# Optimization experiments

Hardware: AMD Instinct MI355X
Metric: run time of the kernel (lower is better)

Reference implementation:

```python
import jax, jax.numpy as jnp
import numpy as np

EMBED_DIM = 768
NUM_HEADS = 12


def setup_inputs() -> dict:
    key = jax.random.key(0)
    ks = jax.random.split(key, 9)
    C = EMBED_DIM
    x = jax.random.normal(ks[0], (8, 3136, C), dtype=jnp.float32)
    s = 0.02
    Wq = jax.random.normal(ks[1], (C, C), dtype=jnp.float32) * s
    Wk = jax.random.normal(ks[2], (C, C), dtype=jnp.float32) * s
    Wv = jax.random.normal(ks[3], (C, C), dtype=jnp.float32) * s
    Wo = jax.random.normal(ks[4], (C, C), dtype=jnp.float32) * s
    bq = jax.random.normal(ks[5], (C,), dtype=jnp.float32) * s
    bk = jax.random.normal(ks[6], (C,), dtype=jnp.float32) * s
    bv = jax.random.normal(ks[7], (C,), dtype=jnp.float32) * s
    bo = jax.random.normal(ks[8], (C,), dtype=jnp.float32) * s
    return {"x": x, "Wq": Wq, "bq": bq, "Wk": Wk, "bk": bk,
            "Wv": Wv, "bv": bv, "Wo": Wo, "bo": bo, "T": 16}


def reference(x, Wq, bq, Wk, bk, Wv, bv, Wo, bo, T):
    B, N, C = x.shape
    H = NUM_HEADS
    hd = C // H
    Hh = H // 2
    P = N // T
    scale = 1.0 / np.sqrt(hd).astype(np.float32)

    Q = (x @ Wq + bq).reshape(B, T, P, H, hd)
    K = (x @ Wk + bk).reshape(B, T, P, H, hd)
    V = (x @ Wv + bv).reshape(B, T, P, H, hd)

    # spatial attention: first Hh heads, attend over patches within each frame
    Qs, Ks, Vs = Q[..., :Hh, :], K[..., :Hh, :], V[..., :Hh, :]
    scores_s = jnp.einsum('btphd,btqhd->bthpq', Qs, Ks) * scale  # (B,T,Hh,P,P)
    ws = jax.nn.softmax(scores_s, axis=-1)
    out_s = jnp.einsum('bthpq,btqhd->btphd', ws, Vs)  # (B,T,P,Hh,hd)

    # temporal attention: last Hh heads, attend over frames at each patch
    Qt, Kt, Vt = Q[..., Hh:, :], K[..., Hh:, :], V[..., Hh:, :]
    scores_t = jnp.einsum('btphd,bsphd->bphts', Qt, Kt) * scale  # (B,P,Hh,T,T)
    wt = jax.nn.softmax(scores_t, axis=-1)
    out_t = jnp.einsum('bphts,bsphd->btphd', wt, Vt)  # (B,T,P,Hh,hd)

    out = jnp.concatenate([out_s, out_t], axis=3).reshape(B, N, C)
    return out @ Wo + bo
```

## Files before the change

### kernel.cpp

```cpp
#include <hip/hip_runtime.h>


typedef __attribute__((ext_vector_type(8))) short short8;
typedef __attribute__((ext_vector_type(4))) float f32x4;

typedef __attribute__((address_space(1))) void gvoid;
typedef __attribute__((address_space(3))) void lvoid;

__device__ __forceinline__ unsigned short f2b(float f) {
  unsigned int u = __float_as_uint(f);
  unsigned int r = (u + 0x7FFFu + ((u >> 16) & 1u)) >> 16;
  return (unsigned short)r;
}

__global__ __launch_bounds__(256) void k_prep(
    const float* __restrict__ x, unsigned short* __restrict__ xb,
    const float* __restrict__ bq, const float* __restrict__ bk,
    const float* __restrict__ bv, float* __restrict__ bqkv,
    const float* __restrict__ Wq, const float* __restrict__ Wk,
    const float* __restrict__ Wv, const float* __restrict__ Wo,
    unsigned short* __restrict__ wqkvT, unsigned short* __restrict__ woT) {
  __shared__ float tile[32][33];
  if (blockIdx.x < 18816) {
    int tid = blockIdx.x * 256 + threadIdx.x;
    if (tid < 2304)
      bqkv[tid] = tid < 768 ? bq[tid] : (tid < 1536 ? bk[tid - 768] : bv[tid - 1536]);
    float4 v = ((const float4*)x)[tid];
    ushort4 o;
    o.x = f2b(v.x); o.y = f2b(v.y); o.z = f2b(v.z); o.w = f2b(v.w);
    ((ushort4*)xb)[tid] = o;
    return;
  }
  int bid = blockIdx.x - 18816;
  const float* W;
  unsigned short* dst;
  int n0, k0;
  if (bid < 1728) {
    int tn = bid % 72, tk = bid / 72;
    n0 = tn * 32; k0 = tk * 32;
    int which = n0 / 768;
    W = which == 0 ? Wq : (which == 1 ? Wk : Wv);
    dst = wqkvT;
  } else {
    int b2 = bid - 1728;
    int tn = b2 % 24, tk = b2 / 24;
    n0 = tn * 32; k0 = tk * 32;
    W = Wo; dst = woT;
  }
  int nn0 = n0 % 768;
  for (int i = threadIdx.x; i < 1024; i += 256) {
    int r = i >> 5, c = i & 31;
    tile[r][c] = W[(size_t)(k0 + r) * 768 + nn0 + c];
  }
  __syncthreads();
  for (int i = threadIdx.x; i < 1024; i += 256) {
    int r = i >> 5, c = i & 31;
    dst[(size_t)(n0 + r) * 768 + k0 + c] = f2b(tile[c][r]);
  }
}


#define FENCE asm volatile("" ::: "memory")
#define BARRIER do { FENCE; __builtin_amdgcn_s_barrier(); FENCE; } while (0)
#define WAIT_LGKM0 asm volatile("s_waitcnt lgkmcnt(0)" ::: "memory")
#define WAIT_VM4 asm volatile("s_waitcnt vmcnt(4)" ::: "memory")

#define STAGE(PBASE, BUFBASE, HT, KT_) do {                                          \
    int kt__ = (KT_);                                                                \
    bool real__ = (kt__ < 12);                                                       \
    if (!real__) kt__ -= 12;                                                         \
    const unsigned short* src__ = (PBASE) + (HT) * 98304 + kt__ * 64;                \
    unsigned d0__ = real__ ? ((BUFBASE) + (HT) * 8192 + w * 512) : (65536u + w * 512); \
    unsigned d1__ = real__ ? ((BUFBASE) + (HT) * 8192 + 4096 + w * 512) : (65536u + w * 512); \
    __builtin_amdgcn_global_load_lds((const gvoid*)src__, (lvoid*)(lds + d0__), 16, 0, 0); \
    __builtin_amdgcn_global_load_lds((const gvoid*)(src__ + 49152), (lvoid*)(lds + d1__), 16, 0, 0); \
  } while (0)

#define LDA(MH, ABASE) do {                                                          \
    const unsigned short* ab__ = lds + (ABASE) + ((MH) * 128 + arow) * 64;           \
    _Pragma("unroll")                                                                \
    for (int mf = 0; mf < 4; ++mf) {                                                 \
      af[mf][0] = *(const short8*)(ab__ + mf * 1024 + s0);                           \
      af[mf][1] = *(const short8*)(ab__ + mf * 1024 + s1);                           \
    }                                                                                \
  } while (0)

#define LDB(NH, BBASE) do {                                                          \
    const unsigned short* bb__ = lds + (BBASE) + ((NH) * 128 + brow) * 64;           \
    _Pragma("unroll")                                                                \
    for (int nf = 0; nf < 2; ++nf) {                                                 \
      bf[nf][0] = *(const short8*)(bb__ + nf * 1024 + s0);                           \
      bf[nf][1] = *(const short8*)(bb__ + nf * 1024 + s1);                           \
    }                                                                                \
  } while (0)

#define MM(MH, NH) do {                                                              \
    __builtin_amdgcn_s_setprio(1);                                                   \
    _Pragma("unroll")                                                                \
    for (int mf = 0; mf < 4; ++mf) {                                                 \
      _Pragma("unroll")                                                              \
      for (int nf = 0; nf < 2; ++nf) {                                               \
        acc[MH][mf][NH][nf] = __builtin_amdgcn_mfma_f32_16x16x32_bf16(               \
            af[mf][0], bf[nf][0], acc[MH][mf][NH][nf], 0, 0, 0);                     \
        acc[MH][mf][NH][nf] = __builtin_amdgcn_mfma_f32_16x16x32_bf16(               \
            af[mf][1], bf[nf][1], acc[MH][mf][NH][nf], 0, 0, 0);                     \
      }                                                                              \
    }                                                                                \
    __builtin_amdgcn_s_setprio(0);                                                   \
  } while (0)

__global__ __launch_bounds__(512, 2) void k_gemm256(
    const unsigned short* __restrict__ A, const unsigned short* __restrict__ Bt,
    const float* __restrict__ bias, unsigned short* __restrict__ Cout,
    int M, int N) {
  __shared__ __align__(16) unsigned short lds[69632];
  const int nwg = gridDim.x;
  const int nbx = N >> 8;
  const int orig = blockIdx.x;
  const int q = nwg >> 3, r = nwg & 7;
  const int xcd = orig & 7, lin = orig >> 3;
  const int wg = (xcd < r ? xcd * (q + 1) : r * (q + 1) + (xcd - r) * q) + lin;
  const int m0 = (wg / nbx) << 8, n0 = (wg % nbx) << 8;

  const int tid = threadIdx.x;
  const int w = tid >> 6, l = tid & 63;
  const int wm = w >> 2, wn = w & 3;
  const int lg = l >> 4, ln = l & 15;
  const int arow = wm * 64 + ln;
  const int brow = wn * 32 + ln;
  const int s0 = (lg ^ (ln & 7)) * 8;
  const int s1 = s0 ^ 32;
  const int srow = tid >> 3;
  const int slg8 = ((tid & 7) ^ (srow & 7)) * 8;
  const unsigned short* pA = A + (size_t)(m0 + srow) * 768 + slg8;
  const unsigned short* pB = Bt + (size_t)(n0 + srow) * 768 + slg8;

  f32x4 acc[2][4][2][2] = {};

  STAGE(pA, 0,     0, 0);
  STAGE(pB, 16384, 0, 0);
  STAGE(pA, 0,     1, 0);
  STAGE(pB, 16384, 1, 0);
  STAGE(pA, 32768, 0, 1);
  STAGE(pB, 49152, 1, 1);
  WAIT_VM4;
  BARRIER;

  for (int it = 0; it < 6; ++it) {
    const int kt1 = 2 * it + 1, ktn0 = 2 * it + 2, ktn1 = 2 * it + 3;
    short8 af[4][2], bf[2][2];
    LDA(0, 0); LDB(0, 16384);
    STAGE(pA, 32768, 1, kt1);
    BARRIER; WAIT_LGKM0; MM(0, 0);
    LDB(1, 16384);
    STAGE(pB, 49152, 0, kt1);
    BARRIER; WAIT_LGKM0; MM(0, 1);
    LDA(1, 0);
    STAGE(pA, 0, 0, ktn0);
    BARRIER; WAIT_LGKM0; MM(1, 1);
    LDB(0, 16384);
    STAGE(pB, 16384, 1, ktn0);
    WAIT_VM4;
    BARRIER; WAIT_LGKM0; MM(1, 0);
    LDA(0, 32768); LDB(0, 49152);
    STAGE(pA, 0, 1, ktn0);
    BARRIER; WAIT_LGKM0; MM(0, 0);
    LDB(1, 49152);
    STAGE(pB, 16384, 0, ktn0);
    BARRIER; WAIT_LGKM0; MM(0, 1);
    LDA(1, 32768);
    STAGE(pA, 32768, 0, ktn1);
    BARRIER; WAIT_LGKM0; MM(1, 1);
    LDB(0, 49152);
    STAGE(pB, 49152, 1, ktn1);
    WAIT_VM4;
    BARRIER; WAIT_LGKM0; MM(1, 0);
  }

#pragma unroll
  for (int mh = 0; mh < 2; ++mh)
#pragma unroll
    for (int mf = 0; mf < 4; ++mf)
#pragma unroll
      for (int nh = 0; nh < 2; ++nh)
#pragma unroll
        for (int nf = 0; nf < 2; ++nf) {
          const int col = n0 + nh * 128 + wn * 32 + nf * 16 + ln;
          const float bval = bias[col];
          const int row = m0 + mh * 128 + wm * 64 + mf * 16 + lg * 4;
#pragma unroll
          for (int rr = 0; rr < 4; ++rr)
            Cout[(size_t)(row + rr) * N + col] = f2b(acc[mh][mf][nh][nf][rr] + bval);
        }
}

__global__ __launch_bounds__(256) void k_gemm_out(
    const unsigned short* __restrict__ A, const unsigned short* __restrict__ Bt,
    const float* __restrict__ bias, float* __restrict__ C,
    int M, int N, int K) {
  __shared__ __align__(16) unsigned short As[2][128 * 32];
  __shared__ __align__(16) unsigned short Bs[2][128 * 32];
  const int tid = threadIdx.x;
  const int w = tid >> 6, l = tid & 63;
  const int lg = l >> 4, ln = l & 15;
  const int m0 = blockIdx.y * 128, n0 = blockIdx.x * 128;
  const int wr = (w >> 1) * 64, wc = (w & 1) * 64;
  f32x4 acc[4][4] = {};
  const unsigned short* ga = A + (size_t)(m0 + (tid >> 2)) * K + ((tid & 3) * 8);
  const unsigned short* gb = Bt + (size_t)(n0 + (tid >> 2)) * K + ((tid & 3) * 8);
  const size_t krow64 = (size_t)64 * K;
  const int wofs = w * 512;

#define OSTAGE(CO, K0) do {                                                                        \
    __builtin_amdgcn_global_load_lds((const gvoid*)(ga + (K0)),          (lvoid*)(&As[0][0] + (CO) + wofs),        16, 0, 0); \
    __builtin_amdgcn_global_load_lds((const gvoid*)(ga + krow64 + (K0)), (lvoid*)(&As[0][0] + (CO) + 2048 + wofs), 16, 0, 0); \
    __builtin_amdgcn_global_load_lds((const gvoid*)(gb + (K0)),          (lvoid*)(&Bs[0][0] + (CO) + wofs),        16, 0, 0); \
    __builtin_amdgcn_global_load_lds((const gvoid*)(gb + krow64 + (K0)), (lvoid*)(&Bs[0][0] + (CO) + 2048 + wofs), 16, 0, 0); \
  } while (0)

  OSTAGE(0, 0);
  asm volatile("s_waitcnt vmcnt(0)" ::: "memory");
  BARRIER;
  int co = 0;
  for (int k0 = 0; k0 < K; k0 += 32) {
    if (k0 + 32 < K) OSTAGE(co ^ 4096, k0 + 32);
    const unsigned short* as = &As[0][0] + co;
    const unsigned short* bs = &Bs[0][0] + co;
    short8 a[4], b[4];
#pragma unroll
    for (int mt = 0; mt < 4; ++mt)
      a[mt] = *(const short8*)(as + (wr + mt * 16 + ln) * 32 + lg * 8);
#pragma unroll
    for (int nt = 0; nt < 4; ++nt)
      b[nt] = *(const short8*)(bs + (wc + nt * 16 + ln) * 32 + lg * 8);
#pragma unroll
    for (int mt = 0; mt < 4; ++mt)
#pragma unroll
      for (int nt = 0; nt < 4; ++nt)
        acc[mt][nt] = __builtin_amdgcn_mfma_f32_16x16x32_bf16(a[mt], b[nt], acc[mt][nt], 0, 0, 0);
    asm volatile("s_waitcnt vmcnt(0)" ::: "memory");
    BARRIER;
    co ^= 4096;
  }
#pragma unroll
  for (int nt = 0; nt < 4; ++nt) {
    int col = n0 + wc + nt * 16 + ln;
    float bval = bias[col];
#pragma unroll
    for (int mt = 0; mt < 4; ++mt) {
      int row = m0 + wr + mt * 16 + lg * 4;
#pragma unroll
      for (int r = 0; r < 4; ++r)
        C[(size_t)(row + r) * N + col] = acc[mt][nt][r] + bval;
    }
  }
#undef OSTAGE
}

__global__ __launch_bounds__(256) void k_attn_fused(
    const unsigned short* __restrict__ qkv, unsigned short* __restrict__ attn) {
  __shared__ __align__(16) unsigned short smem[29696];
  const int w = threadIdx.x >> 6, l = threadIdx.x & 63;
  const int lg = l >> 4, ln = l & 15;
  const float scale = 0.125f;
  if (blockIdx.x < 768) {
    const int bi = blockIdx.x;
    const int h = bi % 6;
    const int t = (bi / 6) % 16;
    const int b = bi / 96;
    const int base_row = b * 3136 + t * 196;
    unsigned short* Vt = smem;
    unsigned short* Pl = smem + 14848;
    for (int i = threadIdx.x; i < 196 * 8; i += 256) {
      int key = i >> 3, d0 = (i & 7) * 8;
      short8 v = *(const short8*)(qkv + (size_t)(base_row + key) * 2304 + 1536 + h * 64 + d0);
#pragma unroll
      for (int j = 0; j < 8; ++j) Vt[(d0 + j) * 232 + key] = (unsigned short)v[j];
    }
    for (int i = threadIdx.x; i < 64 * 28; i += 256)
      Vt[(i / 28) * 232 + 196 + (i % 28)] = 0;
    __syncthreads();
    for (int mt = w; mt < 13; mt += 4) {
      int qm = mt * 16 + ln; if (qm > 195) qm = 195;
      const size_t qoff = (size_t)(base_row + qm) * 2304 + h * 64 + lg * 8;
      short8 qa0 = *(const short8*)(qkv + qoff);
      short8 qa1 = *(const short8*)(qkv + qoff + 32);
      f32x4 st[13];
#pragma unroll
      for (int nt = 0; nt < 13; ++nt) {
        int kn = nt * 16 + ln; if (kn > 195) kn = 195;
        const size_t koff = (size_t)(base_row + kn) * 2304 + 768 + h * 64 + lg * 8;
        short8 kb0 = *(const short8*)(qkv + koff);
        short8 kb1 = *(const short8*)(qkv + koff + 32);
        f32x4 s = {0.f, 0.f, 0.f, 0.f};
        s = __builtin_amdgcn_mfma_f32_16x16x32_bf16(qa0, kb0, s, 0, 0, 0);
        s = __builtin_amdgcn_mfma_f32_16x16x32_bf16(qa1, kb1, s, 0, 0, 0);
        st[nt] = s;
      }
      float mr[4] = {-1e30f, -1e30f, -1e30f, -1e30f};
#pragma unroll
      for (int nt = 0; nt < 13; ++nt) {
        bool valid = (nt * 16 + ln) < 196;
#pragma unroll
        for (int r = 0; r < 4; ++r) {
          float v = valid ? st[nt][r] * scale : -1e30f;
          st[nt][r] = v;
          mr[r] = fmaxf(mr[r], v);
        }
      }
#pragma unroll
      for (int msk = 1; msk <= 8; msk <<= 1)
#pragma unroll
        for (int r = 0; r < 4; ++r) mr[r] = fmaxf(mr[r], __shfl_xor(mr[r], msk));
      float sm[4] = {0.f, 0.f, 0.f, 0.f};
#pragma unroll
      for (int nt = 0; nt < 13; ++nt)
#pragma unroll
        for (int r = 0; r < 4; ++r) {
          float p = __expf(st[nt][r] - mr[r]);
          st[nt][r] = p;
          sm[r] += p;
        }
#pragma unroll
      for (int msk = 1; msk <= 8; msk <<= 1)
#pragma unroll
        for (int r = 0; r < 4; ++r) sm[r] += __shfl_xor(sm[r], msk);
      float inv[4];
#pragma unroll
      for (int r = 0; r < 4; ++r) inv[r] = 1.f / sm[r];
      unsigned short* Pw = Pl + w * 16 * 232;
#pragma unroll
      for (int nt = 0; nt < 13; ++nt)
#pragma unroll
        for (int r = 0; r < 4; ++r)
          Pw[(lg * 4 + r) * 232 + nt * 16 + ln] = f2b(st[nt][r] * inv[r]);
#pragma unroll
      for (int r = 0; r < 4; ++r) Pw[ln * 232 + 208 + lg * 4 + r] = 0;
#pragma unroll
      for (int nt4 = 0; nt4 < 4; ++nt4) {
        f32x4 acc = {0.f, 0.f, 0.f, 0.f};
#pragma unroll
        for (int ks = 0; ks < 7; ++ks) {
          short8 pa = *(const short8*)(Pw + ln * 232 + ks * 32 + lg * 8);
          short8 vb = *(const short8*)(Vt + (nt4 * 16 + ln) * 232 + ks * 32 + lg * 8);
          acc = __builtin_amdgcn_mfma_f32_16x16x32_bf16(pa, vb, acc, 0, 0, 0);
        }
#pragma unroll
        for (int r = 0; r < 4; ++r) {
          int m = mt * 16 + lg * 4 + r;
          if (m < 196)
            attn[(size_t)(base_row + m) * 768 + h * 64 + nt4 * 16 + ln] = f2b(acc[r]);
        }
      }
    }
  } else {
    const int u = (blockIdx.x - 768) * 4 + w;
    const int b = u / 1176;
    const int rem = u % 1176;
    const int p = rem / 6;
    const int h = 6 + rem % 6;
    const size_t rowb = (size_t)b * 3136 + p;
    unsigned short* Vt = smem + w * 2560;
    unsigned short* Pl = smem + 10240 + w * 640;
    for (int i = l; i < 128; i += 64) {
      int tt = i >> 3, d0 = (i & 7) * 8;
      short8 v = *(const short8*)(qkv + (rowb + (size_t)tt * 196) * 2304 + 1536 + h * 64 + d0);
#pragma unroll
      for (int j = 0; j < 8; ++j) Vt[(d0 + j) * 40 + tt] = (unsigned short)v[j];
    }
    for (int i = l; i < 1024; i += 64)
      Vt[(i >> 4) * 40 + 16 + (i & 15)] = 0;
    const size_t qoff = (rowb + (size_t)ln * 196) * 2304 + h * 64 + lg * 8;
    short8 qa0 = *(const short8*)(qkv + qoff);
    short8 qa1 = *(const short8*)(qkv + qoff + 32);
    short8 kb0 = *(const short8*)(qkv + qoff + 768);
    short8 kb1 = *(const short8*)(qkv + qoff + 768 + 32);
    f32x4 s = {0.f, 0.f, 0.f, 0.f};
    s = __builtin_amdgcn_mfma_f32_16x16x32_bf16(qa0, kb0, s, 0, 0, 0);
    s = __builtin_amdgcn_mfma_f32_16x16x32_bf16(qa1, kb1, s, 0, 0, 0);
    float stv[4], mr[4];
#pragma unroll
    for (int r = 0; r < 4; ++r) { stv[r] = s[r] * scale; mr[r] = stv[r]; }
#pragma unroll
    for (int msk = 1; msk <= 8; msk <<= 1)
#pragma unroll
      for (int r = 0; r < 4; ++r) mr[r] = fmaxf(mr[r], __shfl_xor(mr[r], msk));
    float sm[4];
#pragma unroll
    for (int r = 0; r < 4; ++r) { stv[r] = __expf(stv[r] - mr[r]); sm[r] = stv[r]; }
#pragma unroll
    for (int msk = 1; msk <= 8; msk <<= 1)
#pragma unroll
      for (int r = 0; r < 4; ++r) sm[r] += __shfl_xor(sm[r], msk);
#pragma unroll
    for (int r = 0; r < 4; ++r)
      Pl[(lg * 4 + r) * 40 + ln] = f2b(stv[r] / sm[r]);
#pragma unroll
    for (int r = 0; r < 4; ++r) Pl[ln * 40 + 16 + lg * 4 + r] = 0;
    short8 pa = *(const short8*)(Pl + ln * 40 + lg * 8);
#pragma unroll
    for (int nt4 = 0; nt4 < 4; ++nt4) {
      short8 vb = *(const short8*)(Vt + (nt4 * 16 + ln) * 40 + lg * 8);
      f32x4 acc = {0.f, 0.f, 0.f, 0.f};
      acc = __builtin_amdgcn_mfma_f32_16x16x32_bf16(pa, vb, acc, 0, 0, 0);
#pragma unroll
      for (int r = 0; r < 4; ++r) {
        int tq = lg * 4 + r;
        attn[((size_t)b * 3136 + (size_t)tq * 196 + p) * 768 + h * 64 + nt4 * 16 + ln] = f2b(acc[r]);
      }
    }
  }
}

extern "C" void kernel_launch(void* const* d_in, const int* in_sizes, int n_in,
                              void* d_out, int out_size, void* d_ws, size_t ws_size,
                              hipStream_t stream) {
  const float* x  = (const float*)d_in[0];
  const float* Wq = (const float*)d_in[1];
  const float* bq = (const float*)d_in[2];
  const float* Wk = (const float*)d_in[3];
  const float* bk = (const float*)d_in[4];
  const float* Wv = (const float*)d_in[5];
  const float* bv = (const float*)d_in[6];
  const float* Wo = (const float*)d_in[7];
  const float* bo = (const float*)d_in[8];
  float* out = (float*)d_out;
  char* ws = (char*)d_ws;
  unsigned short* xb    = (unsigned short*)(ws + 0);
  unsigned short* wqkvT = (unsigned short*)(ws + 38535168);
  float*          bqkv  = (float*)(ws + 42074112);
  unsigned short* woT   = (unsigned short*)(ws + 42083328);
  unsigned short* qkvb  = (unsigned short*)(ws + 43262976);
  unsigned short* attnb = (unsigned short*)(ws + 158868480);

  k_prep<<<21120, 256, 0, stream>>>(x, xb, bq, bk, bv, bqkv, Wq, Wk, Wv, Wo, wqkvT, woT);
  k_gemm256<<<882, 512, 0, stream>>>(xb, wqkvT, bqkv, qkvb, 25088, 2304);
  k_attn_fused<<<3120, 256, 0, stream>>>(qkvb, attnb);
  k_gemm_out<<<dim3(6, 196), 256, 0, stream>>>(attnb, woT, bo, out, 25088, 768, 768);
}
```

Baseline: 248.3 us.

## Keep softmax probabilities in registers by transposing QK^T and permuting V layout

Computes S^T (K as the A operand, Q as the B operand) so each lane's MFMA accumulator maps directly onto the A-operand register layout of the PV MFMA. V columns in shared memory are permuted to match that layout. This removes the shared-memory round trip for P and halves the kernel's LDS footprint. It also drops the max subtraction from softmax and defers normalization to the output, which saves the reductions but risks overflow in exp when scores are large.

```diff
diff --git a/kernel.cpp b/kernel.cpp
--- a/kernel.cpp
+++ b/kernel.cpp
@@ -1,8 +1,10 @@
 #include <hip/hip_runtime.h>
+#include <hip/hip_bf16.h>
 
 
 typedef __attribute__((ext_vector_type(8))) short short8;
 typedef __attribute__((ext_vector_type(4))) float f32x4;
+typedef __attribute__((ext_vector_type(4))) unsigned int u32x4;
 
 typedef __attribute__((address_space(1))) void gvoid;
 typedef __attribute__((address_space(3))) void lvoid;
@@ -11,6 +13,18 @@
   unsigned int u = __float_as_uint(f);
   unsigned int r = (u + 0x7FFFu + ((u >> 16) & 1u)) >> 16;
   return (unsigned short)r;
+}
+
+__device__ __forceinline__ unsigned int pk2(float a, float b) {
+  union { __hip_bfloat162 h; unsigned int u; } cv;
+  cv.h = __float22bfloat162_rn(float2{a, b});
+  return cv.u;
+}
+
+__device__ __forceinline__ int vperm(int key) {
+  int u = key & 31;
+  return (key & ~31) | (((u >> 3) & 1) << 4) | (((u >> 2) & 1) << 3) |
+         (((u >> 4) & 1) << 2) | (u & 3);
 }
 
 __global__ __launch_bounds__(256) void k_prep(
@@ -259,7 +273,7 @@
 
 __global__ __launch_bounds__(256) void k_attn_fused(
     const unsigned short* __restrict__ qkv, unsigned short* __restrict__ attn) {
-  __shared__ __align__(16) unsigned short smem[29696];
+  __shared__ __align__(16) unsigned short smem[14848];
   const int w = threadIdx.x >> 6, l = threadIdx.x & 63;
   const int lg = l >> 4, ln = l & 15;
   const float scale = 0.125f;
@@ -270,12 +284,12 @@
     const int b = bi / 96;
     const int base_row = b * 3136 + t * 196;
     unsigned short* Vt = smem;
-    unsigned short* Pl = smem + 14848;
     for (int i = threadIdx.x; i < 196 * 8; i += 256) {
       int key = i >> 3, d0 = (i & 7) * 8;
       short8 v = *(const short8*)(qkv + (size_t)(base_row + key) * 2304 + 1536 + h * 64 + d0);
-#pragma unroll
-      for (int j = 0; j < 8; ++j) Vt[(d0 + j) * 232 + key] = (unsigned short)v[j];
+      int col = vperm(key);
+#pragma unroll
+      for (int j = 0; j < 8; ++j) Vt[(d0 + j) * 232 + col] = (unsigned short)v[j];
     }
     for (int i = threadIdx.x; i < 64 * 28; i += 256)
       Vt[(i / 28) * 232 + 196 + (i % 28)] = 0;
@@ -283,73 +297,63 @@
     for (int mt = w; mt < 13; mt += 4) {
       int qm = mt * 16 + ln; if (qm > 195) qm = 195;
       const size_t qoff = (size_t)(base_row + qm) * 2304 + h * 64 + lg * 8;
-      short8 qa0 = *(const short8*)(qkv + qoff);
-      short8 qa1 = *(const short8*)(qkv + qoff + 32);
+      short8 qb0 = *(const short8*)(qkv + qoff);
+      short8 qb1 = *(const short8*)(qkv + qoff + 32);
       f32x4 st[13];
 #pragma unroll
       for (int nt = 0; nt < 13; ++nt) {
         int kn = nt * 16 + ln; if (kn > 195) kn = 195;
         const size_t koff = (size_t)(base_row + kn) * 2304 + 768 + h * 64 + lg * 8;
-        short8 kb0 = *(const short8*)(qkv + koff);
-        short8 kb1 = *(const short8*)(qkv + koff + 32);
+        short8 ka0 = *(const short8*)(qkv + koff);
+        short8 ka1 = *(const short8*)(qkv + koff + 32);
         f32x4 s = {0.f, 0.f, 0.f, 0.f};
-        s = __builtin_amdgcn_mfma_f32_16x16x32_bf16(qa0, kb0, s, 0, 0, 0);
-        s = __builtin_amdgcn_mfma_f32_16x16x32_bf16(qa1, kb1, s, 0, 0, 0);
+        s = __builtin_amdgcn_mfma_f32_16x16x32_bf16(ka0, qb0, s, 0, 0, 0);
+        s = __builtin_amdgcn_mfma_f32_16x16x32_bf16(ka1, qb1, s, 0, 0, 0);
         st[nt] = s;
       }
-      float mr[4] = {-1e30f, -1e30f, -1e30f, -1e30f};
-#pragma unroll
-      for (int nt = 0; nt < 13; ++nt) {
-        bool valid = (nt * 16 + ln) < 196;
+      float sum = 0.f;
+#pragma unroll
+      for (int nt = 0; nt < 13; ++nt)
 #pragma unroll
         for (int r = 0; r < 4; ++r) {
-          float v = valid ? st[nt][r] * scale : -1e30f;
-          st[nt][r] = v;
-          mr[r] = fmaxf(mr[r], v);
+          bool valid = (nt * 16 + lg * 4 + r) < 196;
+          float p = valid ? __expf(st[nt][r] * scale) : 0.f;
+          st[nt][r] = p;
+          sum += p;
         }
+      sum += __shfl_xor(sum, 16);
+      sum += __shfl_xor(sum, 32);
+      float inv = 1.f / sum;
+      float invR[4];
+#pragma unroll
+      for (int r = 0; r < 4; ++r) invR[r] = __shfl(inv, lg * 4 + r);
+      short8 pa[7];
+#pragma unroll
+      for (int ks = 0; ks < 7; ++ks) {
+        union { u32x4 u; short8 s; } pb;
+        pb.u[0] = pk2(st[2 * ks][0], st[2 * ks][1]);
+        pb.u[1] = pk2(st[2 * ks][2], st[2 * ks][3]);
+        if (ks < 6) {
+          pb.u[2] = pk2(st[2 * ks + 1][0], st[2 * ks + 1][1]);
+          pb.u[3] = pk2(st[2 * ks + 1][2], st[2 * ks + 1][3]);
+        } else {
+          pb.u[2] = 0; pb.u[3] = 0;
+        }
+        pa[ks] = pb.s;
       }
-#pragma unroll
-      for (int msk = 1; msk <= 8; msk <<= 1)
-#pragma unroll
-        for (int r = 0; r < 4; ++r) mr[r] = fmaxf(mr[r], __shfl_xor(mr[r], msk));
-      float sm[4] = {0.f, 0.f, 0.f, 0.f};
-#pragma unroll
-      for (int nt = 0; nt < 13; ++nt)
-#pragma unroll
-        for (int r = 0; r < 4; ++r) {
-          float p = __expf(st[nt][r] - mr[r]);
-          st[nt][r] = p;
-          sm[r] += p;
-        }
-#pragma unroll
-      for (int msk = 1; msk <= 8; msk <<= 1)
-#pragma unroll
-        for (int r = 0; r < 4; ++r) sm[r] += __shfl_xor(sm[r], msk);
-      float inv[4];
-#pragma unroll
-      for (int r = 0; r < 4; ++r) inv[r] = 1.f / sm[r];
-      unsigned short* Pw = Pl + w * 16 * 232;
-#pragma unroll
-      for (int nt = 0; nt < 13; ++nt)
-#pragma unroll
-        for (int r = 0; r < 4; ++r)
-          Pw[(lg * 4 + r) * 232 + nt * 16 + ln] = f2b(st[nt][r] * inv[r]);
-#pragma unroll
-      for (int r = 0; r < 4; ++r) Pw[ln * 232 + 208 + lg * 4 + r] = 0;
 #pragma unroll
       for (int nt4 = 0; nt4 < 4; ++nt4) {
         f32x4 acc = {0.f, 0.f, 0.f, 0.f};
 #pragma unroll
         for (int ks = 0; ks < 7; ++ks) {
-          short8 pa = *(const short8*)(Pw + ln * 232 + ks * 32 + lg * 8);
           short8 vb = *(const short8*)(Vt + (nt4 * 16 + ln) * 232 + ks * 32 + lg * 8);
-          acc = __builtin_amdgcn_mfma_f32_16x16x32_bf16(pa, vb, acc, 0, 0, 0);
+          acc = __builtin_amdgcn_mfma_f32_16x16x32_bf16(pa[ks], vb, acc, 0, 0, 0);
         }
 #pragma unroll
         for (int r = 0; r < 4; ++r) {
           int m = mt * 16 + lg * 4 + r;
           if (m < 196)
-            attn[(size_t)(base_row + m) * 768 + h * 64 + nt4 * 16 + ln] = f2b(acc[r]);
+            attn[(size_t)(base_row + m) * 768 + h * 64 + nt4 * 16 + ln] = f2b(acc[r] * invR[r]);
         }
       }
     }
@@ -361,52 +365,49 @@
     const int h = 6 + rem % 6;
     const size_t rowb = (size_t)b * 3136 + p;
     unsigned short* Vt = smem + w * 2560;
-    unsigned short* Pl = smem + 10240 + w * 640;
     for (int i = l; i < 128; i += 64) {
       int tt = i >> 3, d0 = (i & 7) * 8;
       short8 v = *(const short8*)(qkv + (rowb + (size_t)tt * 196) * 2304 + 1536 + h * 64 + d0);
-#pragma unroll
-      for (int j = 0; j < 8; ++j) Vt[(d0 + j) * 40 + tt] = (unsigned short)v[j];
-    }
-    for (int i = l; i < 1024; i += 64)
-      Vt[(i >> 4) * 40 + 16 + (i & 15)] = 0;
+      int col = (((tt >> 3) & 1) << 4) | (((tt >> 2) & 1) << 3) | (tt & 3);
+#pragma unroll
+      for (int j = 0; j < 8; ++j) Vt[(d0 + j) * 40 + col] = (unsigned short)v[j];
+    }
+    for (int i = l; i < 1024; i += 64) {
+      int d = i >> 4, c = i & 15;
+      Vt[d * 40 + (((c >> 2) << 3) + 4 + (c & 3))] = 0;
+    }
     const size_t qoff = (rowb + (size_t)ln * 196) * 2304 + h * 64 + lg * 8;
-    short8 qa0 = *(const short8*)(qkv + qoff);
-    short8 qa1 = *(const short8*)(qkv + qoff + 32);
-    short8 kb0 = *(const short8*)(qkv + qoff + 768);
-    short8 kb1 = *(const short8*)(qkv + qoff + 768 + 32);
+    short8 qb0 = *(const short8*)(qkv + qoff);
+    short8 qb1 = *(const short8*)(qkv + qoff + 32);
+    short8 ka0 = *(const short8*)(qkv + qoff + 768);
+    short8 ka1 = *(const short8*)(qkv + qoff + 768 + 32);
     f32x4 s = {0.f, 0.f, 0.f, 0.f};
-    s = __builtin_amdgcn_mfma_f32_16x16x32_bf16(qa0, kb0, s, 0, 0, 0);
-    s = __builtin_amdgcn_mfma_f32_16x16x32_bf16(qa1, kb1, s, 0, 0, 0);
-    float stv[4], mr[4];
-#pragma unroll
-    for (int r = 0; r < 4; ++r) { stv[r] = s[r] * scale; mr[r] = stv[r]; }
-#pragma unroll
-    for (int msk = 1; msk <= 8; msk <<= 1)
-#pragma unroll
-      for (int r = 0; r < 4; ++r) mr[r] = fmaxf(mr[r], __shfl_xor(mr[r], msk));
-    float sm[4];
-#pragma unroll
-    for (int r = 0; r < 4; ++r) { stv[r] = __expf(stv[r] - mr[r]); sm[r] = stv[r]; }
-#pragma unroll
-    for (int msk = 1; msk <= 8; msk <<= 1)
-#pragma unroll
-      for (int r = 0; r < 4; ++r) sm[r] += __shfl_xor(sm[r], msk);
-#pragma unroll
-    for (int r = 0; r < 4; ++r)
-      Pl[(lg * 4 + r) * 40 + ln] = f2b(stv[r] / sm[r]);
-#pragma unroll
-    for (int r = 0; r < 4; ++r) Pl[ln * 40 + 16 + lg * 4 + r] = 0;
-    short8 pa = *(const short8*)(Pl + ln * 40 + lg * 8);
+    s = __builtin_amdgcn_mfma_f32_16x16x32_bf16(ka0, qb0, s, 0, 0, 0);
+    s = __builtin_amdgcn_mfma_f32_16x16x32_bf16(ka1, qb1, s, 0, 0, 0);
+    float pv[4];
+    float sum = 0.f;
+#pragma unroll
+    for (int r = 0; r < 4; ++r) { pv[r] = __expf(s[r] * scale); sum += pv[r]; }
+    sum += __shfl_xor(sum, 16);
+    sum += __shfl_xor(sum, 32);
+    float inv = 1.f / sum;
+    float invR[4];
+#pragma unroll
+    for (int r = 0; r < 4; ++r) invR[r] = __shfl(inv, lg * 4 + r);
+    union { u32x4 u; short8 s; } pb;
+    pb.u[0] = pk2(pv[0], pv[1]);
+    pb.u[1] = pk2(pv[2], pv[3]);
+    pb.u[2] = 0; pb.u[3] = 0;
 #pragma unroll
     for (int nt4 = 0; nt4 < 4; ++nt4) {
       short8 vb = *(const short8*)(Vt + (nt4 * 16 + ln) * 40 + lg * 8);
       f32x4 acc = {0.f, 0.f, 0.f, 0.f};
-      acc = __builtin_amdgcn_mfma_f32_16x16x32_bf16(pa, vb, acc, 0, 0, 0);
+      acc = __builtin_amdgcn_mfma_f32_16x16x32_bf16(pb.s, vb, acc, 0, 0, 0);
 #pragma unroll
       for (int r = 0; r < 4; ++r) {
         int tq = lg * 4 + r;
-        attn[((size_t)b * 3136 + (size_t)tq * 196 + p) * 768 + h * 64 + nt4 * 16 + ln] = f2b(acc[r]);
+        attn[((size_t)b * 3136 + (size_t)tq * 196 + p) * 768 + h * 64 + nt4 * 16 + ln] =
+            f2b(acc[r] * invR[r]);
       }
     }
   }
```

After: 260.1 us. 4.8% more time.

## Triple-buffer output GEMM loads and XOR-swizzle LDS layout

Applied to the files above, without the earlier changes.

The output projection GEMM moves from double to triple buffering, keeping two K-tiles of global-to-LDS loads in flight and waiting with a partial vmcnt rather than draining every load. When no real tile remains, dummy loads go to a scratch LDS region so the outstanding-load count stays uniform. The 16-byte chunk placement within each row is also XOR-swizzled by row to cut LDS bank conflicts on the fragment reads. In exchange the kernel uses more LDS, which may lower occupancy, and issues a few wasted loads at the tail.

```diff
diff --git a/kernel.cpp b/kernel.cpp
--- a/kernel.cpp
+++ b/kernel.cpp
@@ -198,49 +198,56 @@
     const unsigned short* __restrict__ A, const unsigned short* __restrict__ Bt,
     const float* __restrict__ bias, float* __restrict__ C,
     int M, int N, int K) {
-  __shared__ __align__(16) unsigned short As[2][128 * 32];
-  __shared__ __align__(16) unsigned short Bs[2][128 * 32];
+  __shared__ __align__(16) unsigned short lds[26624];
   const int tid = threadIdx.x;
   const int w = tid >> 6, l = tid & 63;
   const int lg = l >> 4, ln = l & 15;
   const int m0 = blockIdx.y * 128, n0 = blockIdx.x * 128;
   const int wr = (w >> 1) * 64, wc = (w & 1) * 64;
   f32x4 acc[4][4] = {};
-  const unsigned short* ga = A + (size_t)(m0 + (tid >> 2)) * K + ((tid & 3) * 8);
-  const unsigned short* gb = Bt + (size_t)(n0 + (tid >> 2)) * K + ((tid & 3) * 8);
+  const int srow = tid >> 2;
+  const int sg = ((tid & 3) ^ (srow & 3)) * 8;
+  const unsigned short* ga = A + (size_t)(m0 + srow) * K + sg;
+  const unsigned short* gb = Bt + (size_t)(n0 + srow) * K + sg;
   const size_t krow64 = (size_t)64 * K;
   const int wofs = w * 512;
-
-#define OSTAGE(CO, K0) do {                                                                        \
-    __builtin_amdgcn_global_load_lds((const gvoid*)(ga + (K0)),          (lvoid*)(&As[0][0] + (CO) + wofs),        16, 0, 0); \
-    __builtin_amdgcn_global_load_lds((const gvoid*)(ga + krow64 + (K0)), (lvoid*)(&As[0][0] + (CO) + 2048 + wofs), 16, 0, 0); \
-    __builtin_amdgcn_global_load_lds((const gvoid*)(gb + (K0)),          (lvoid*)(&Bs[0][0] + (CO) + wofs),        16, 0, 0); \
-    __builtin_amdgcn_global_load_lds((const gvoid*)(gb + krow64 + (K0)), (lvoid*)(&Bs[0][0] + (CO) + 2048 + wofs), 16, 0, 0); \
+  const int rs = (lg ^ (ln & 3)) * 8;
+
+#define OSTAGE3(BUF, K0, REAL) do {                                                                \
+    int k__ = (REAL) ? (K0) : 0;                                                                   \
+    unsigned a__ = (REAL) ? ((unsigned)(BUF) * 8192u + wofs) : (24576u + wofs);                    \
+    unsigned b__ = (REAL) ? ((unsigned)(BUF) * 8192u + 4096u + wofs) : (24576u + wofs);            \
+    __builtin_amdgcn_global_load_lds((const gvoid*)(ga + k__),          (lvoid*)(lds + a__),        16, 0, 0); \
+    __builtin_amdgcn_global_load_lds((const gvoid*)(ga + krow64 + k__), (lvoid*)(lds + a__ + 2048), 16, 0, 0); \
+    __builtin_amdgcn_global_load_lds((const gvoid*)(gb + k__),          (lvoid*)(lds + b__),        16, 0, 0); \
+    __builtin_amdgcn_global_load_lds((const gvoid*)(gb + krow64 + k__), (lvoid*)(lds + b__ + 2048), 16, 0, 0); \
   } while (0)
 
-  OSTAGE(0, 0);
-  asm volatile("s_waitcnt vmcnt(0)" ::: "memory");
+  OSTAGE3(0, 0, true);
+  OSTAGE3(1, 32, true);
+  WAIT_VM4;
   BARRIER;
-  int co = 0;
-  for (int k0 = 0; k0 < K; k0 += 32) {
-    if (k0 + 32 < K) OSTAGE(co ^ 4096, k0 + 32);
-    const unsigned short* as = &As[0][0] + co;
-    const unsigned short* bs = &Bs[0][0] + co;
+  int bcur = 0, bnxt = 1, bpre = 2;
+  const int nk = K >> 5;
+  for (int i = 0; i < nk; ++i) {
+    OSTAGE3(bpre, (i + 2) * 32, i + 2 < nk);
+    const unsigned short* as = lds + bcur * 8192;
+    const unsigned short* bs = as + 4096;
     short8 a[4], b[4];
 #pragma unroll
     for (int mt = 0; mt < 4; ++mt)
-      a[mt] = *(const short8*)(as + (wr + mt * 16 + ln) * 32 + lg * 8);
+      a[mt] = *(const short8*)(as + (wr + mt * 16 + ln) * 32 + rs);
 #pragma unroll
     for (int nt = 0; nt < 4; ++nt)
-      b[nt] = *(const short8*)(bs + (wc + nt * 16 + ln) * 32 + lg * 8);
+      b[nt] = *(const short8*)(bs + (wc + nt * 16 + ln) * 32 + rs);
 #pragma unroll
     for (int mt = 0; mt < 4; ++mt)
 #pragma unroll
       for (int nt = 0; nt < 4; ++nt)
         acc[mt][nt] = __builtin_amdgcn_mfma_f32_16x16x32_bf16(a[mt], b[nt], acc[mt][nt], 0, 0, 0);
-    asm volatile("s_waitcnt vmcnt(0)" ::: "memory");
+    WAIT_VM4;
     BARRIER;
-    co ^= 4096;
+    int t = bcur; bcur = bnxt; bnxt = bpre; bpre = t;
   }
 #pragma unroll
   for (int nt = 0; nt < 4; ++nt) {
@@ -254,7 +261,7 @@
         C[(size_t)(row + r) * N + col] = acc[mt][nt][r] + bval;
     }
   }
-#undef OSTAGE
+#undef OSTAGE3
 }
 
 __global__ __launch_bounds__(256) void k_attn_fused(
```

Result: no change. 247.4 us (-0.4%).
